# Kernel optimization log

Hardware: AMD Instinct MI355X
Metric: run time of the kernel (lower is better)

The kernel has to match this reference:

```python
import jax, jax.numpy as jnp
import numpy as np

EPS = 1e-5

def _ln(x):
    m = jnp.mean(x, axis=-1, keepdims=True)
    v = jnp.mean((x - m) ** 2, axis=-1, keepdims=True)
    return (x - m) / jnp.sqrt(v + EPS)

def setup_inputs() -> dict:
    key = jax.random.key(0)
    ks = jax.random.split(key, 6)
    B, S, E, H = 2, 2048, 1024, 16
    sd = 1.0 / np.sqrt(E)
    x = jax.random.normal(ks[0], (B, S, E), dtype=jnp.float32)
    w_in = jax.random.normal(ks[1], (3 * E, E), dtype=jnp.float32) * sd
    w_out = jax.random.normal(ks[2], (E, E), dtype=jnp.float32) * sd
    w_fc = jax.random.normal(ks[3], (4 * E, E), dtype=jnp.float32) * sd
    b_fc = jnp.zeros((4 * E,), dtype=jnp.float32)
    w_proj = jax.random.normal(ks[4], (E, 4 * E), dtype=jnp.float32) * (1.0 / np.sqrt(4 * E))
    b_proj = jnp.zeros((E,), dtype=jnp.float32)
    return {"x": x, "w_in": w_in, "w_out": w_out, "w_fc": w_fc,
            "b_fc": b_fc, "w_proj": w_proj, "b_proj": b_proj}

def reference(x, w_in, w_out, w_fc, b_fc, w_proj, b_proj):
    B, S, E = x.shape
    H = 16
    D = E // H
    h = _ln(x)
    qkv = h @ w_in.T                      # [B,S,3E]
    q, k, v = jnp.split(qkv, 3, axis=-1)
    q = q.reshape(B, S, H, D)
    k = k.reshape(B, S, H, D)
    v = v.reshape(B, S, H, D)
    scale = 1.0 / np.sqrt(D)
    scores = jnp.einsum('bqhd,bkhd->bhqk', q, k) * scale  # [B,H,S,S]
    causal = jnp.tril(jnp.ones((S, S), dtype=bool))
    scores = jnp.where(causal, scores, -jnp.inf)
    attn = jax.nn.softmax(scores, axis=-1)
    o = jnp.einsum('bhqk,bkhd->bqhd', attn, v).reshape(B, S, E)
    attn_out = o @ w_out.T
    x2 = x + attn_out                      # residual 1
    h2 = _ln(x2)
    m = jax.nn.relu(h2 @ w_fc.T + b_fc)    # [B,S,4E]
    return (m @ w_proj.T + b_proj) + x2    # residual 2
```

## Files before the change

kernel.cpp:

```cpp
#include <hip/hip_runtime.h>
#include <stdint.h>

#define AS1 __attribute__((address_space(1)))
#define AS3 __attribute__((address_space(3)))

typedef __bf16 bf8_t __attribute__((ext_vector_type(8)));
typedef float f4_t __attribute__((ext_vector_type(4)));
typedef unsigned short ush;

__device__ __forceinline__ ush f2b(float f) {
  unsigned u = __builtin_bit_cast(unsigned, f);
  u += 0x7fffu + ((u >> 16) & 1u);
  return (ush)(u >> 16);
}
__device__ __forceinline__ void unpack8(uint4 u, float* dst) {
  unsigned a0 = u.x, a1 = u.y, a2 = u.z, a3 = u.w;
  dst[0] = __builtin_bit_cast(float, a0 << 16);
  dst[1] = __builtin_bit_cast(float, a0 & 0xffff0000u);
  dst[2] = __builtin_bit_cast(float, a1 << 16);
  dst[3] = __builtin_bit_cast(float, a1 & 0xffff0000u);
  dst[4] = __builtin_bit_cast(float, a2 << 16);
  dst[5] = __builtin_bit_cast(float, a2 & 0xffff0000u);
  dst[6] = __builtin_bit_cast(float, a3 << 16);
  dst[7] = __builtin_bit_cast(float, a3 & 0xffff0000u);
}

__global__ __launch_bounds__(256) void f2b_all(
    const float* __restrict__ w_in, const float* __restrict__ w_out,
    const float* __restrict__ w_fc, const float* __restrict__ w_proj,
    ush* __restrict__ o_in, ush* __restrict__ o_out,
    ush* __restrict__ o_fc, ush* __restrict__ o_proj) {
  const int blk = blockIdx.x;
  const float* src;
  ush* dst;
  int base;
  if (blk < 3072) { src = w_in; dst = o_in; base = blk; }
  else if (blk < 4096) { src = w_out; dst = o_out; base = blk - 3072; }
  else if (blk < 8192) { src = w_fc; dst = o_fc; base = blk - 4096; }
  else { src = w_proj; dst = o_proj; base = blk - 8192; }
  const int i = (base * 256 + threadIdx.x) * 4;
  float4 v = *(const float4*)(src + i);
  union { ush u[4]; uint2 d; } p;
  p.u[0] = f2b(v.x); p.u[1] = f2b(v.y); p.u[2] = f2b(v.z); p.u[3] = f2b(v.w);
  *(uint2*)(dst + i) = p.d;
}

__global__ __launch_bounds__(256) void ln_kernel(const float* __restrict__ x,
                                                 ush* __restrict__ out) {
  const int row = blockIdx.x, tid = threadIdx.x;
  const float* xr = x + (size_t)row * 1024;
  float4 v = ((const float4*)xr)[tid];
  float s = v.x + v.y + v.z + v.w;
  float q = v.x * v.x + v.y * v.y + v.z * v.z + v.w * v.w;
  for (int o = 32; o; o >>= 1) { s += __shfl_down(s, o); q += __shfl_down(q, o); }
  __shared__ float rs[4], rq[4];
  const int w = tid >> 6;
  if ((tid & 63) == 0) { rs[w] = s; rq[w] = q; }
  __syncthreads();
  s = rs[0] + rs[1] + rs[2] + rs[3];
  q = rq[0] + rq[1] + rq[2] + rq[3];
  const float mean = s * (1.0f / 1024.0f);
  const float var = q * (1.0f / 1024.0f) - mean * mean;
  const float rstd = rsqrtf(var + 1e-5f);
  union { ush u[4]; uint2 d; } p;
  p.u[0] = f2b((v.x - mean) * rstd);
  p.u[1] = f2b((v.y - mean) * rstd);
  p.u[2] = f2b((v.z - mean) * rstd);
  p.u[3] = f2b((v.w - mean) * rstd);
  *(uint2*)(out + (size_t)row * 1024 + tid * 4) = p.d;
}

template <int EPI, int BM, int MINW>
__global__ __launch_bounds__(256, MINW) void gemm_bt(
    const ush* __restrict__ A, const ush* __restrict__ Bw,
    int M, int N, int K,
    const float* __restrict__ bias, const float* __restrict__ resid,
    float* __restrict__ outF, ush* __restrict__ outB) {
  constexpr int MI = BM / 32;
  constexpr int NCH = (BM + 128) / 16;
  constexpr int PC = NCH / 4;
  constexpr int ASZ = BM * 32;
  __shared__ ush lds[2 * ASZ + 2 * 4096];
  const int tid = threadIdx.x;
  const int wave = tid >> 6, lane = tid & 63;
  const int bm = blockIdx.x, bn = blockIdx.y;
  const int wm = (wave & 1) * (BM / 2), wn = (wave >> 1) * 64;
  const int l16 = lane & 15, quad = lane >> 4;
  const int srow = lane >> 2;
  const int scol = (lane & 3) * 8;

  const ush* Abase = A + (size_t)(bm * BM) * K;
  const ush* Bbase = Bw + (size_t)(bn * 128) * K;

  f4_t acc[MI][4];
#pragma unroll
  for (int i = 0; i < MI; ++i)
#pragma unroll
    for (int j = 0; j < 4; ++j) acc[i][j] = (f4_t){0.f, 0.f, 0.f, 0.f};

  const int kiters = K >> 5;

  auto stage = [&](int k0, int buf) {
    const int kk = k0 * 32;
#pragma unroll
    for (int i = 0; i < PC; ++i) {
      const int c = wave * PC + i;
      if (c < BM / 16) {
        const ush* ga = Abase + (size_t)(c * 16 + srow) * K + kk + scol;
        __builtin_amdgcn_global_load_lds((const AS1 void*)ga,
                                         (AS3 void*)(lds + buf * ASZ + c * 512), 16, 0, 0);
      } else {
        const int c2 = c - BM / 16;
        const ush* gb = Bbase + (size_t)(c2 * 16 + srow) * K + kk + scol;
        __builtin_amdgcn_global_load_lds(
            (const AS1 void*)gb, (AS3 void*)(lds + 2 * ASZ + buf * 4096 + c2 * 512), 16, 0, 0);
      }
    }
  };

  stage(0, 0);
  __syncthreads();
  for (int k0 = 0; k0 < kiters; ++k0) {
    const int cur = k0 & 1;
    if (k0 + 1 < kiters) stage(k0 + 1, cur ^ 1);
    bf8_t af[MI], bfr[4];
#pragma unroll
    for (int mi = 0; mi < MI; ++mi)
      af[mi] = *(const bf8_t*)&lds[cur * ASZ + (wm + mi * 16 + l16) * 32 + quad * 8];
#pragma unroll
    for (int ni = 0; ni < 4; ++ni)
      bfr[ni] = *(const bf8_t*)&lds[2 * ASZ + cur * 4096 + (wn + ni * 16 + l16) * 32 + quad * 8];
#pragma unroll
    for (int mi = 0; mi < MI; ++mi)
#pragma unroll
      for (int ni = 0; ni < 4; ++ni)
        acc[mi][ni] =
            __builtin_amdgcn_mfma_f32_16x16x32_bf16(af[mi], bfr[ni], acc[mi][ni], 0, 0, 0);
    __syncthreads();
  }

  if (EPI == 0 || EPI == 2) {
    ush* eb = lds + wave * ASZ;
#pragma unroll
    for (int mi = 0; mi < MI; ++mi)
#pragma unroll
      for (int ni = 0; ni < 4; ++ni) {
        const int gn = bn * 128 + wn + ni * 16 + l16;
        const float bv = (EPI == 2) ? bias[gn] : 0.0f;
#pragma unroll
        for (int r = 0; r < 4; ++r) {
          float v = acc[mi][ni][r] + bv;
          if (EPI == 2) v = fmaxf(v, 0.0f);
          eb[(mi * 16 + quad * 4 + r) * 64 + ni * 16 + l16] = f2b(v);
        }
      }
#pragma unroll
    for (int j = 0; j < BM / 16; ++j) {
      const int lr = j * 8 + (lane >> 3);
      const int c8 = (lane & 7) * 8;
      uint4 v = *(const uint4*)&eb[lr * 64 + c8];
      *(uint4*)(outB + (size_t)(bm * BM + wm + lr) * N + bn * 128 + wn + c8) = v;
    }
  } else {
#pragma unroll
    for (int mi = 0; mi < MI; ++mi) {
#pragma unroll
      for (int ni = 0; ni < 4; ++ni) {
        const int gm0 = bm * BM + wm + mi * 16 + quad * 4;
        const int gn = bn * 128 + wn + ni * 16 + l16;
        const float bv = (EPI == 3) ? bias[gn] : 0.0f;
#pragma unroll
        for (int r = 0; r < 4; ++r) {
          const size_t idx = (size_t)(gm0 + r) * N + gn;
          outF[idx] = acc[mi][ni][r] + bv + resid[idx];
        }
      }
    }
  }
}

__global__ __launch_bounds__(256) void pack_kv(const ush* __restrict__ qkv,
                                               ush* __restrict__ Kp,
                                               ush* __restrict__ Vp) {
  const int lin = blockIdx.x;
  const int kt = lin & 31, h = (lin >> 5) & 15, b = lin >> 9;
  const int tid = threadIdx.x;
  __shared__ ush Vs[64 * 72];
  const size_t rowbase = (size_t)(b * 2048 + kt * 64) * 3072 + h * 64;
  ush* Kt = Kp + (size_t)lin * 4096;
  ush* Vt = Vp + (size_t)lin * 4096;

  const int r0 = tid >> 3, cin = tid & 7;
#pragma unroll
  for (int it = 0; it < 2; ++it) {
    const int r = r0 + it * 32;
    uint4 ku = *(const uint4*)(qkv + rowbase + (size_t)r * 3072 + 1024 + cin * 8);
    float f[8]; unpack8(ku, f);
    union { ush us[8]; uint4 v; } pk;
#pragma unroll
    for (int j = 0; j < 8; ++j) pk.us[j] = f2b(f[j] * 0.125f);
    *(uint4*)(Kt + (size_t)(r * 8 + (cin ^ (r & 7))) * 8) = pk.v;
    uint4 vu = *(const uint4*)(qkv + rowbase + (size_t)r * 3072 + 2048 + cin * 8);
    *(uint4*)&Vs[r * 72 + cin * 8] = vu;
  }
  __syncthreads();
#pragma unroll
  for (int oc2 = 0; oc2 < 2; ++oc2) {
    const int oc = tid * 2 + oc2;
    const int d = oc >> 3, c = oc & 7;
    const int k0 = 8 * (c ^ (d & 7));
    union { ush us[8]; uint4 v; } pk;
#pragma unroll
    for (int j = 0; j < 8; ++j) pk.us[j] = Vs[(k0 + j) * 72 + d];
    *(uint4*)(Vt + (size_t)oc * 8) = pk.v;
  }
}

__global__ __launch_bounds__(256, 4) void attn_kernel(const ush* __restrict__ qkv,
                                                      const ush* __restrict__ Kp,
                                                      const ush* __restrict__ Vp,
                                                      ush* __restrict__ o) {
  const int lin = blockIdx.x;
  const int b = lin & 1, h = (lin >> 1) & 15, tq = lin >> 5;
  const int tid = threadIdx.x;
  const int wave = tid >> 6, lane = tid & 63;
  const int l15 = lane & 15, quad = lane >> 4;

  __shared__ __align__(16) ush Ks[64 * 64];
  __shared__ __align__(16) ush Vt[64 * 64];
  __shared__ __align__(16) ush Ps[64 * 72];

  bf8_t qf[2];
  {
    const int qrow = b * 2048 + tq * 64 + wave * 16 + l15;
#pragma unroll
    for (int s = 0; s < 2; ++s) {
      union { uint4 u; bf8_t v; } pk;
      pk.u = *(const uint4*)(qkv + (size_t)qrow * 3072 + h * 64 + s * 32 + quad * 8);
      qf[s] = pk.v;
    }
  }

  float m_s = -1e30f, l_s = 0.f;
  f4_t O[4];
#pragma unroll
  for (int j = 0; j < 4; ++j) O[j] = (f4_t){0.f, 0.f, 0.f, 0.f};

  const int qw0 = tq * 64 + wave * 16;
  const int swz = (l15 & 7) * 8;
  const size_t tile0 = (size_t)((b * 16 + h) * 32) * 4096;

  for (int kt = 0; kt <= tq; ++kt) {
    __syncthreads();
    const ush* Ktile = Kp + tile0 + (size_t)kt * 4096;
    const ush* Vtile = Vp + tile0 + (size_t)kt * 4096;
#pragma unroll
    for (int i = 0; i < 2; ++i) {
      const int seg = wave * 2 + i;
      __builtin_amdgcn_global_load_lds((const AS1 void*)(Ktile + seg * 512 + lane * 8),
                                       (AS3 void*)(Ks + seg * 512), 16, 0, 0);
      __builtin_amdgcn_global_load_lds((const AS1 void*)(Vtile + seg * 512 + lane * 8),
                                       (AS3 void*)(Vt + seg * 512), 16, 0, 0);
    }
    __syncthreads();

    f4_t S[4];
#pragma unroll
    for (int mi = 0; mi < 4; ++mi) S[mi] = (f4_t){0.f, 0.f, 0.f, 0.f};
#pragma unroll
    for (int s = 0; s < 2; ++s)
#pragma unroll
      for (int mi = 0; mi < 4; ++mi) {
        bf8_t kf = *(const bf8_t*)&Ks[(mi * 16 + l15) * 64 + (((4 * s + quad) * 8) ^ swz)];
        S[mi] = __builtin_amdgcn_mfma_f32_16x16x32_bf16(kf, qf[s], S[mi], 0, 0, 0);
      }

    if (kt == tq) {
#pragma unroll
      for (int mi = 0; mi < 4; ++mi)
#pragma unroll
        for (int r = 0; r < 4; ++r) {
          const int kg = kt * 64 + mi * 16 + quad * 4 + r;
          const int qg = qw0 + l15;
          if (kg > qg) S[mi][r] = -1e30f;
        }
    }

    float mx = -1e30f;
#pragma unroll
    for (int mi = 0; mi < 4; ++mi)
#pragma unroll
      for (int r = 0; r < 4; ++r) mx = fmaxf(mx, S[mi][r]);
    mx = fmaxf(mx, __shfl_xor(mx, 16));
    mx = fmaxf(mx, __shfl_xor(mx, 32));
    const float mn = fmaxf(m_s, mx);
    const float alpha = __expf(m_s - mn);
    float sum = 0.f;
#pragma unroll
    for (int mi = 0; mi < 4; ++mi)
#pragma unroll
      for (int r = 0; r < 4; ++r) {
        const float p = __expf(S[mi][r] - mn);
        S[mi][r] = p;
        sum += p;
      }
    sum += __shfl_xor(sum, 16);
    sum += __shfl_xor(sum, 32);
    m_s = mn;
    l_s = l_s * alpha + sum;
#pragma unroll
    for (int mi = 0; mi < 4; ++mi) {
      uint2 w2;
      w2.x = (unsigned)f2b(S[mi][0]) | ((unsigned)f2b(S[mi][1]) << 16);
      w2.y = (unsigned)f2b(S[mi][2]) | ((unsigned)f2b(S[mi][3]) << 16);
      *(uint2*)&Ps[(wave * 16 + l15) * 72 + mi * 16 + quad * 4] = w2;
    }

    bf8_t pf[2], vf[4][2];
#pragma unroll
    for (int s = 0; s < 2; ++s)
      pf[s] = *(const bf8_t*)&Ps[(wave * 16 + l15) * 72 + s * 32 + quad * 8];
#pragma unroll
    for (int n4 = 0; n4 < 4; ++n4)
#pragma unroll
      for (int s = 0; s < 2; ++s)
        vf[n4][s] = *(const bf8_t*)&Vt[(n4 * 16 + l15) * 64 + (((4 * s + quad) * 8) ^ swz)];
    float ar[4];
#pragma unroll
    for (int r = 0; r < 4; ++r) ar[r] = __shfl(alpha, quad * 4 + r);
#pragma unroll
    for (int n4 = 0; n4 < 4; ++n4) {
#pragma unroll
      for (int r = 0; r < 4; ++r) O[n4][r] *= ar[r];
#pragma unroll
      for (int s = 0; s < 2; ++s)
        O[n4] = __builtin_amdgcn_mfma_f32_16x16x32_bf16(pf[s], vf[n4][s], O[n4], 0, 0, 0);
    }
  }

  const float rc = 1.0f / l_s;
  float rr[4];
#pragma unroll
  for (int r = 0; r < 4; ++r) rr[r] = __shfl(rc, quad * 4 + r);
#pragma unroll
  for (int n4 = 0; n4 < 4; ++n4)
#pragma unroll
    for (int r = 0; r < 4; ++r) {
      const int qg = tq * 64 + wave * 16 + quad * 4 + r;
      o[(size_t)(b * 2048 + qg) * 1024 + h * 64 + n4 * 16 + l15] = f2b(O[n4][r] * rr[r]);
    }
}

extern "C" void kernel_launch(void* const* d_in, const int* in_sizes, int n_in,
                              void* d_out, int out_size, void* d_ws, size_t ws_size,
                              hipStream_t stream) {
  const float* x = (const float*)d_in[0];
  const float* w_in = (const float*)d_in[1];
  const float* w_out = (const float*)d_in[2];
  const float* w_fc = (const float*)d_in[3];
  const float* b_fc = (const float*)d_in[4];
  const float* w_proj = (const float*)d_in[5];
  const float* b_proj = (const float*)d_in[6];
  float* out = (float*)d_out;

  char* ws = (char*)d_ws;
  ush* w_in_b = (ush*)(ws);
  ush* w_out_b = (ush*)(ws + 6291456);
  ush* w_fc_b = (ush*)(ws + 8388608);
  ush* w_proj_b = (ush*)(ws + 16777216);
  ush* h_b = (ush*)(ws + 25165824);
  float* x2 = (float*)(ws + 33554432);
  ush* qkv_b = (ush*)(ws + 50331648);
  ush* o_b = (ush*)(ws + 75497472);
  ush* m_b = (ush*)(ws + 50331648);
  ush* Kp = (ush*)(ws + 83886080);
  ush* Vp = (ush*)(ws + 92274688);

  f2b_all<<<12288, 256, 0, stream>>>(w_in, w_out, w_fc, w_proj,
                                     w_in_b, w_out_b, w_fc_b, w_proj_b);

  ln_kernel<<<4096, 256, 0, stream>>>(x, h_b);

  gemm_bt<0, 128, 2><<<dim3(32, 24), 256, 0, stream>>>(
      h_b, w_in_b, 4096, 3072, 1024, nullptr, nullptr, nullptr, qkv_b);

  pack_kv<<<1024, 256, 0, stream>>>(qkv_b, Kp, Vp);

  attn_kernel<<<1024, 256, 0, stream>>>(qkv_b, Kp, Vp, o_b);

  gemm_bt<1, 64, 4><<<dim3(64, 8), 256, 0, stream>>>(
      o_b, w_out_b, 4096, 1024, 1024, nullptr, x, x2, nullptr);

  ln_kernel<<<4096, 256, 0, stream>>>(x2, h_b);

  gemm_bt<2, 128, 2><<<dim3(32, 32), 256, 0, stream>>>(
      h_b, w_fc_b, 4096, 4096, 1024, b_fc, nullptr, nullptr, m_b);

  gemm_bt<3, 64, 4><<<dim3(64, 8), 256, 0, stream>>>(
      m_b, w_proj_b, 4096, 1024, 4096, b_proj, x2, out, nullptr);
}
```

Before: 338.3 us.

## Add 256x256-tile 8-wave pipelined GEMM for QKV and FC projections

Introduces a new GEMM kernel with 512 threads and 256x256 output tiles. It stages half-tiles through async global-to-LDS loads into double buffers with XOR swizzling, interleaves those loads between MFMA sub-steps, and raises wave priority during the MFMA phases. The kernel replaces the 128-row gemm_bt for the QKV and FC GEMMs to increase data reuse per block and overlap loads with compute. In exchange it uses 128KB of LDS and large accumulator register files, and launches only 192 and 256 blocks, which may underfill the 256 CUs and limit occupancy.

```diff
diff --git a/kernel.cpp b/kernel.cpp
--- a/kernel.cpp
+++ b/kernel.cpp
@@ -70,6 +70,182 @@
   *(uint2*)(out + (size_t)row * 1024 + tid * 4) = p.d;
 }
 
+template <int EPI>
+__global__ __launch_bounds__(512, 2) void gemm8p(
+    const ush* __restrict__ A, const ush* __restrict__ Bw,
+    int M, int N, int K,
+    const float* __restrict__ bias, const float* __restrict__ resid,
+    float* __restrict__ outF, ush* __restrict__ outB) {
+  __shared__ __align__(16) ush lds[65536];
+  ush* const LA0 = lds;
+  ush* const LA1 = lds + 16384;
+  ush* const LB0 = lds + 32768;
+  ush* const LB1 = lds + 49152;
+
+  const int tid = threadIdx.x;
+  const int wave = tid >> 6, lane = tid & 63;
+  const int wm = wave >> 2, wn = wave & 3;
+  const int l16 = lane & 15, quad = lane >> 4;
+  const int sw = l16 & 7;
+  const int bm = blockIdx.x, bn = blockIdx.y;
+  const int bmrow = bm * 256, bnrow = bn * 256;
+  const int KT = K >> 6;
+  const int nit = KT >> 1;
+  const int gcs = (((lane & 7) ^ ((lane >> 3) & 7)) << 3);
+
+  auto stage = [&](const ush* __restrict__ gbase, int blkrow, ush* dstbase,
+                   int t, int h) {
+    const int kt = t & (KT - 1);
+#pragma unroll
+    for (int i2 = 0; i2 < 2; ++i2) {
+      const int rr = h * 128 + (wave * 2 + i2) * 8 + (lane >> 3);
+      const ush* g = gbase + (size_t)(blkrow + rr) * K + kt * 64 + gcs;
+      __builtin_amdgcn_global_load_lds(
+          (const AS1 void*)g,
+          (AS3 void*)(dstbase + h * 8192 + (wave * 2 + i2) * 512), 16, 0, 0);
+    }
+  };
+
+  f4_t acc[8][4];
+#pragma unroll
+  for (int i = 0; i < 8; ++i)
+#pragma unroll
+    for (int j = 0; j < 4; ++j) acc[i][j] = (f4_t){0.f, 0.f, 0.f, 0.f};
+
+  stage(A, bmrow, LA0, 0, 0);
+  stage(A, bmrow, LA0, 0, 1);
+  stage(Bw, bnrow, LB0, 0, 0);
+  stage(Bw, bnrow, LB0, 0, 1);
+  stage(A, bmrow, LA1, 1, 0);
+  asm volatile("s_waitcnt vmcnt(2)" ::: "memory");
+  __builtin_amdgcn_s_barrier();
+
+  bf8_t af[4][2], bf[2][2];
+
+  for (int it = 0; it < nit; ++it) {
+#pragma unroll
+    for (int hf = 0; hf < 2; ++hf) {
+      ush* const cA = hf ? LA1 : LA0;
+      ush* const cB = hf ? LB1 : LB0;
+#pragma unroll
+      for (int sub = 0; sub < 4; ++sub) {
+        const int p = hf * 4 + sub;
+        if (sub == 0) {
+#pragma unroll
+          for (int m = 0; m < 4; ++m)
+#pragma unroll
+            for (int kk = 0; kk < 2; ++kk)
+              af[m][kk] = *(const bf8_t*)&cA[(wm * 128 + m * 16 + l16) * 64 +
+                                            (((kk * 4 + quad) ^ sw) << 3)];
+#pragma unroll
+          for (int n = 0; n < 2; ++n)
+#pragma unroll
+            for (int kk = 0; kk < 2; ++kk)
+              bf[n][kk] = *(const bf8_t*)&cB[(wn * 64 + n * 16 + l16) * 64 +
+                                            (((kk * 4 + quad) ^ sw) << 3)];
+        } else if (sub == 1) {
+#pragma unroll
+          for (int n = 0; n < 2; ++n)
+#pragma unroll
+            for (int kk = 0; kk < 2; ++kk)
+              bf[n][kk] = *(const bf8_t*)&cB[(wn * 64 + (2 + n) * 16 + l16) * 64 +
+                                            (((kk * 4 + quad) ^ sw) << 3)];
+        } else if (sub == 2) {
+#pragma unroll
+          for (int m = 0; m < 4; ++m)
+#pragma unroll
+            for (int kk = 0; kk < 2; ++kk)
+              af[m][kk] = *(const bf8_t*)&cA[(wm * 128 + (4 + m) * 16 + l16) * 64 +
+                                            (((kk * 4 + quad) ^ sw) << 3)];
+#pragma unroll
+          for (int n = 0; n < 2; ++n)
+#pragma unroll
+            for (int kk = 0; kk < 2; ++kk)
+              bf[n][kk] = *(const bf8_t*)&cB[(wn * 64 + n * 16 + l16) * 64 +
+                                            (((kk * 4 + quad) ^ sw) << 3)];
+        } else {
+#pragma unroll
+          for (int n = 0; n < 2; ++n)
+#pragma unroll
+            for (int kk = 0; kk < 2; ++kk)
+              bf[n][kk] = *(const bf8_t*)&cB[(wn * 64 + (2 + n) * 16 + l16) * 64 +
+                                            (((kk * 4 + quad) ^ sw) << 3)];
+        }
+        if (p == 0) stage(A, bmrow, LA1, 2 * it + 1, 1);
+        else if (p == 1) stage(Bw, bnrow, LB1, 2 * it + 1, 0);
+        else if (p == 2) stage(Bw, bnrow, LB1, 2 * it + 1, 1);
+        else if (p == 3) stage(A, bmrow, LA0, 2 * it + 2, 0);
+        else if (p == 4) stage(A, bmrow, LA0, 2 * it + 2, 1);
+        else if (p == 5) stage(Bw, bnrow, LB0, 2 * it + 2, 0);
+        else if (p == 6) stage(Bw, bnrow, LB0, 2 * it + 2, 1);
+        else stage(A, bmrow, LA1, 2 * it + 3, 0);
+        if (sub == 3) asm volatile("s_waitcnt vmcnt(2)" ::: "memory");
+        __builtin_amdgcn_s_barrier();
+        asm volatile("s_waitcnt lgkmcnt(0)" ::: "memory");
+        __builtin_amdgcn_sched_barrier(0);
+        __builtin_amdgcn_s_setprio(1);
+        const int mo = (sub >= 2) ? 4 : 0;
+        const int no = (sub & 1) ? 2 : 0;
+#pragma unroll
+        for (int m = 0; m < 4; ++m)
+#pragma unroll
+          for (int n = 0; n < 2; ++n)
+#pragma unroll
+            for (int kk = 0; kk < 2; ++kk)
+              acc[mo + m][no + n] = __builtin_amdgcn_mfma_f32_16x16x32_bf16(
+                  af[m][kk], bf[n][kk], acc[mo + m][no + n], 0, 0, 0);
+        __builtin_amdgcn_s_setprio(0);
+        __builtin_amdgcn_s_barrier();
+      }
+    }
+  }
+
+  asm volatile("s_waitcnt vmcnt(0)" ::: "memory");
+  __builtin_amdgcn_s_barrier();
+
+  if (EPI == 0 || EPI == 2) {
+    ush* eb = lds + wave * 8192;
+    float bv[4];
+    if (EPI == 2) {
+#pragma unroll
+      for (int ni = 0; ni < 4; ++ni) bv[ni] = bias[bn * 256 + wn * 64 + ni * 16 + l16];
+    }
+#pragma unroll
+    for (int mi = 0; mi < 8; ++mi)
+#pragma unroll
+      for (int ni = 0; ni < 4; ++ni)
+#pragma unroll
+        for (int r = 0; r < 4; ++r) {
+          float v = acc[mi][ni][r];
+          if (EPI == 2) v = fmaxf(v + bv[ni], 0.0f);
+          eb[(mi * 16 + quad * 4 + r) * 64 + ni * 16 + l16] = f2b(v);
+        }
+    asm volatile("s_waitcnt lgkmcnt(0)" ::: "memory");
+#pragma unroll
+    for (int j = 0; j < 16; ++j) {
+      const int lr = j * 8 + (lane >> 3);
+      const int c8 = (lane & 7) * 8;
+      uint4 v = *(const uint4*)&eb[lr * 64 + c8];
+      *(uint4*)(outB + (size_t)(bm * 256 + wm * 128 + lr) * N + bn * 256 +
+                wn * 64 + c8) = v;
+    }
+  } else {
+#pragma unroll
+    for (int mi = 0; mi < 8; ++mi)
+#pragma unroll
+      for (int ni = 0; ni < 4; ++ni) {
+        const int gm0 = bm * 256 + wm * 128 + mi * 16 + quad * 4;
+        const int gn = bn * 256 + wn * 64 + ni * 16 + l16;
+        const float bv = (EPI == 3) ? bias[gn] : 0.0f;
+#pragma unroll
+        for (int r = 0; r < 4; ++r) {
+          const size_t idx = (size_t)(gm0 + r) * N + gn;
+          outF[idx] = acc[mi][ni][r] + bv + resid[idx];
+        }
+      }
+  }
+}
+
 template <int EPI, int BM, int MINW>
 __global__ __launch_bounds__(256, MINW) void gemm_bt(
     const ush* __restrict__ A, const ush* __restrict__ Bw,
@@ -381,7 +557,7 @@
 
   ln_kernel<<<4096, 256, 0, stream>>>(x, h_b);
 
-  gemm_bt<0, 128, 2><<<dim3(32, 24), 256, 0, stream>>>(
+  gemm8p<0><<<dim3(16, 12), 512, 0, stream>>>(
       h_b, w_in_b, 4096, 3072, 1024, nullptr, nullptr, nullptr, qkv_b);
 
   pack_kv<<<1024, 256, 0, stream>>>(qkv_b, Kp, Vp);
@@ -393,7 +569,7 @@
 
   ln_kernel<<<4096, 256, 0, stream>>>(x2, h_b);
 
-  gemm_bt<2, 128, 2><<<dim3(32, 32), 256, 0, stream>>>(
+  gemm8p<2><<<dim3(16, 16), 512, 0, stream>>>(
       h_b, w_fc_b, 4096, 4096, 1024, b_fc, nullptr, nullptr, m_b);
 
   gemm_bt<3, 64, 4><<<dim3(64, 8), 256, 0, stream>>>(
```

Result: faster. 328.7 us (-2.8%).
